# Optimization experiments

Measured on AMD Instinct MI355X. Metric: run time of the kernel, lower is better.

## Reference

```python
import jax, jax.numpy as jnp
import numpy as np

B, NQ, NKV = 4, 1024, 2048
Q_DIM = K_DIM = V_DIM = 1024
HEADS, DIM_HEAD = 16, 64
INNER = HEADS * DIM_HEAD


def setup_inputs() -> dict:
    key = jax.random.key(0)
    ks = jax.random.split(key, 10)
    return {
        "x": jax.random.normal(ks[0], (B, NQ, Q_DIM), dtype=jnp.float32),
        "key_t": jax.random.normal(ks[1], (B, NKV, K_DIM), dtype=jnp.float32),
        "value": jax.random.normal(ks[2], (B, NKV, V_DIM), dtype=jnp.float32),
        "mask": jax.random.randint(ks[3], (B, NQ, NKV), 0, 2) == 1,
        "Wq": jax.random.normal(ks[4], (Q_DIM, INNER), dtype=jnp.float32) * (Q_DIM ** -0.5),
        "Wk": jax.random.normal(ks[5], (K_DIM, INNER), dtype=jnp.float32) * (K_DIM ** -0.5),
        "Wv": jax.random.normal(ks[6], (V_DIM, INNER), dtype=jnp.float32) * (V_DIM ** -0.5),
        "Wo": jax.random.normal(ks[7], (INNER, Q_DIM), dtype=jnp.float32) * (INNER ** -0.5),
        "gamma": jnp.ones((Q_DIM,), dtype=jnp.float32),
        "beta": jnp.zeros((Q_DIM,), dtype=jnp.float32),
    }


def reference(x, key_t, value, mask, Wq, Wk, Wv, Wo, gamma, beta):
    # LayerNorm over last dim
    mu = jnp.mean(x, axis=-1, keepdims=True)
    var = jnp.var(x, axis=-1, keepdims=True)
    xn = (x - mu) * jax.lax.rsqrt(var + 1e-5) * gamma + beta

    h, d = HEADS, DIM_HEAD
    # b n (h d) -> b h n d
    q = (xn @ Wq).reshape(B, NQ, h, d).transpose(0, 2, 1, 3)
    k = (key_t @ Wk).reshape(B, NKV, h, d).transpose(0, 2, 1, 3)
    v = (value @ Wv).reshape(B, NKV, h, d).transpose(0, 2, 1, 3)

    scale = d ** -0.5
    dots = jnp.einsum("bhnd,bhmd->bhnm", q, k) * scale  # [b,h,nq,nkv]
    min_neg = -jnp.finfo(dots.dtype).max
    dots = jnp.where(mask[:, None, :, :], min_neg, dots)
    attn = jax.nn.softmax(dots, axis=-1)
    out = jnp.einsum("bhnm,bhmd->bhnd", attn, v)
    out = out.transpose(0, 2, 1, 3).reshape(B, NQ, INNER)  # b h n d -> b n (h d)
    return out @ Wo
```

## Files before the change

kernel.cpp:

```cpp
#include <hip/hip_runtime.h>

typedef unsigned short u16;
typedef unsigned int u32;
typedef unsigned char u8;

typedef __attribute__((ext_vector_type(8))) short bf16x8;
typedef __attribute__((ext_vector_type(4))) short bf16x4;
typedef __attribute__((ext_vector_type(4))) float f32x4;

__device__ __forceinline__ float bf2f(u16 u) {
    union { u32 i; float f; } v; v.i = ((u32)u) << 16; return v.f;
}
__device__ __forceinline__ u16 f2bf(float f) {
    union { float f; u32 i; } v; v.f = f;
    u32 r = v.i + 0x7fffu + ((v.i >> 16) & 1u);
    return (u16)(r >> 16);
}
__device__ __forceinline__ u32 pkbf(float a, float b) {
    return (u32)f2bf(a) | ((u32)f2bf(b) << 16);
}
__device__ __forceinline__ float fexp2(float x) { return __builtin_amdgcn_exp2f(x); }

__device__ __forceinline__ void async16(u16* lds, const u16* g) {
    __builtin_amdgcn_global_load_lds(
        (const __attribute__((address_space(1))) void*)g,
        (__attribute__((address_space(3))) void*)lds, 16, 0, 0);
}

__global__ __launch_bounds__(256) void detect_dtype(const u32* __restrict__ x,
                                                    int* __restrict__ flag) {
    int tid = threadIdx.x;
    int hits = 0;
    for (int i = 0; i < 4; ++i) {
        u32 w = x[tid * 4 + i];
        u32 e = (w >> 7) & 0xFFu;
        hits += (e >= 110u && e <= 131u) ? 1 : 0;
    }
    for (int off = 1; off < 64; off <<= 1) hits += __shfl_xor(hits, off, 64);
    __shared__ int red[4];
    int wave = tid >> 6, lane = tid & 63;
    if (lane == 0) red[wave] = hits;
    __syncthreads();
    if (tid == 0) flag[0] = (red[0] + red[1] + red[2] + red[3] > 512) ? 1 : 0;
}

__global__ __launch_bounds__(256) void conv_bf16_2(const void* __restrict__ src0,
                                                   const void* __restrict__ src1,
                                                   u16* __restrict__ dst0,
                                                   u16* __restrict__ dst1,
                                                   const int* __restrict__ flagp,
                                                   int half_blocks) {
    int flag = *flagp;
    const void* src = (blockIdx.x < (u32)half_blocks) ? src0 : src1;
    u16* dst = (blockIdx.x < (u32)half_blocks) ? dst0 : dst1;
    int blk = (blockIdx.x < (u32)half_blocks) ? blockIdx.x : (blockIdx.x - half_blocks);
    size_t i = (size_t)blk * 256 + threadIdx.x;
    if (flag) {
        ((uint4*)dst)[i] = ((const uint4*)src)[i];
    } else {
        const float4* s = (const float4*)src + i * 2;
        float4 f0 = s[0], f1 = s[1];
        u16 t[8];
        t[0] = f2bf(f0.x); t[1] = f2bf(f0.y); t[2] = f2bf(f0.z); t[3] = f2bf(f0.w);
        t[4] = f2bf(f1.x); t[5] = f2bf(f1.y); t[6] = f2bf(f1.z); t[7] = f2bf(f1.w);
        ((uint4*)dst)[i] = *(const uint4*)t;
    }
}

__global__ __launch_bounds__(256) void mask_pack(const int* __restrict__ m,
                                                 u8* __restrict__ o) {
    size_t i = (size_t)blockIdx.x * 256 + threadIdx.x;
    const int4* mp = (const int4*)m + i * 4;
    uint4 out;
    u32* op = (u32*)&out;
    for (int j = 0; j < 4; ++j) {
        int4 a = mp[j];
        op[j] = (a.x == 0 ? 0xFFu : 0u) | (a.y == 0 ? 0xFF00u : 0u) |
                (a.z == 0 ? 0xFF0000u : 0u) | (a.w == 0 ? 0xFF000000u : 0u);
    }
    ((uint4*)o)[i] = out;
}

__global__ __launch_bounds__(256) void ln_kernel(const void* __restrict__ x_,
                                                 const void* __restrict__ g_,
                                                 const void* __restrict__ b_,
                                                 u16* __restrict__ out,
                                                 const int* __restrict__ flagp) {
    int flag = *flagp;
    int row = blockIdx.x;
    int tid = threadIdx.x;
    float v[4];
    if (flag) {
        const u16* xr = (const u16*)x_ + (size_t)row * 1024;
        uint2 d = *(const uint2*)&xr[tid * 4];
        v[0] = bf2f((u16)(d.x & 0xffff));
        v[1] = bf2f((u16)(d.x >> 16));
        v[2] = bf2f((u16)(d.y & 0xffff));
        v[3] = bf2f((u16)(d.y >> 16));
    } else {
        const float* xr = (const float*)x_ + (size_t)row * 1024;
        float4 d = *(const float4*)&xr[tid * 4];
        v[0] = d.x; v[1] = d.y; v[2] = d.z; v[3] = d.w;
    }
    float s  = v[0] + v[1] + v[2] + v[3];
    float ss = v[0]*v[0] + v[1]*v[1] + v[2]*v[2] + v[3]*v[3];
    for (int off = 1; off < 64; off <<= 1) {
        s  += __shfl_xor(s,  off, 64);
        ss += __shfl_xor(ss, off, 64);
    }
    __shared__ float red[8];
    int wave = tid >> 6, lane = tid & 63;
    if (lane == 0) { red[wave] = s; red[4 + wave] = ss; }
    __syncthreads();
    s  = red[0] + red[1] + red[2] + red[3];
    ss = red[4] + red[5] + red[6] + red[7];
    float mu   = s * (1.0f / 1024.0f);
    float var  = ss * (1.0f / 1024.0f) - mu * mu;
    float rstd = rsqrtf(var + 1e-5f);
    u16 r01[4];
    for (int j = 0; j < 4; ++j) {
        float g, bb;
        if (flag) { g = bf2f(((const u16*)g_)[tid * 4 + j]); bb = bf2f(((const u16*)b_)[tid * 4 + j]); }
        else      { g = ((const float*)g_)[tid * 4 + j];     bb = ((const float*)b_)[tid * 4 + j]; }
        r01[j] = f2bf((v[j] - mu) * rstd * g + bb);
    }
    uint2 o;
    o.x = (u32)r01[0] | ((u32)r01[1] << 16);
    o.y = (u32)r01[2] | ((u32)r01[3] << 16);
    *(uint2*)&out[(size_t)row * 1024 + tid * 4] = o;
}

__global__ __launch_bounds__(256) void transpose64x4(const void* __restrict__ s0,
                                                     const void* __restrict__ s1,
                                                     const void* __restrict__ s2,
                                                     const void* __restrict__ s3,
                                                     u16* __restrict__ d0,
                                                     u16* __restrict__ d1,
                                                     u16* __restrict__ d2,
                                                     u16* __restrict__ d3,
                                                     int rows, int cols,
                                                     const int* __restrict__ flagp) {
    __shared__ u16 t[64][65];
    int flag = *flagp;
    const void* src_ = (blockIdx.z == 0) ? s0 : (blockIdx.z == 1) ? s1 :
                       (blockIdx.z == 2) ? s2 : s3;
    u16* dst = (blockIdx.z == 0) ? d0 : (blockIdx.z == 1) ? d1 :
               (blockIdx.z == 2) ? d2 : d3;
    int bx = blockIdx.x * 64;
    int by = blockIdx.y * 64;
    int tid = threadIdx.x;
    for (int i = 0; i < 16; ++i) {
        int r = i * 4 + (tid >> 6);
        int c = tid & 63;
        size_t idx = (size_t)(by + r) * cols + bx + c;
        t[r][c] = flag ? ((const u16*)src_)[idx] : f2bf(((const float*)src_)[idx]);
    }
    __syncthreads();
    for (int i = 0; i < 16; ++i) {
        int r = i * 4 + (tid >> 6);
        int c = tid & 63;
        dst[(size_t)(bx + r) * rows + by + c] = t[c][r];
    }
}

__global__ __launch_bounds__(256, 2) void gemm128(const u16* __restrict__ A,
                                                  const u16* __restrict__ Bt,
                                                  void* __restrict__ C_,
                                                  int M, int N, int K,
                                                  const int* __restrict__ flagp,
                                                  int c_flagged, float cscale,
                                                  int vt_mode, int mdiv) {
    __shared__ u16 As[128 * 64];
    __shared__ u16 Bs[128 * 64];
    int flag = *flagp;
    bool c_bf16 = c_flagged ? (flag != 0) : true;

    int id  = blockIdx.x;
    int j   = id >> 3;
    int gy  = (id & 7) + 8 * (j % mdiv);
    int bnt = j / mdiv;

    int tid  = threadIdx.x;
    int wave = tid >> 6, lane = tid & 63;
    int quad = lane >> 4, l16 = lane & 15;
    size_t bm = (size_t)gy * 128;
    size_t bn = (size_t)bnt * 128;
    int wm = (wave >> 1) * 64, wn = (wave & 1) * 64;

    int lr  = lane >> 3;
    int csw = (lane & 7) ^ lr;
    const u16* Ag = A  + (bm + wave * 32 + lr) * (size_t)K + csw * 8;
    const u16* Bg = Bt + (bn + wave * 32 + lr) * (size_t)K + csw * 8;
    u16* Al = &As[(wave * 32) * 64];
    u16* Bl = &Bs[(wave * 32) * 64];

    f32x4 acc[4][4];
#pragma unroll
    for (int i = 0; i < 4; ++i)
#pragma unroll
        for (int jj = 0; jj < 4; ++jj)
            acc[i][jj] = (f32x4){0.f, 0.f, 0.f, 0.f};

    int rsw = l16 & 7;

    for (int k0 = 0; k0 < K; k0 += 64) {
        __syncthreads();
#pragma unroll
        for (int i = 0; i < 4; ++i) {
            async16(Al + i * 8 * 64, Ag + (size_t)i * 8 * K + k0);
            async16(Bl + i * 8 * 64, Bg + (size_t)i * 8 * K + k0);
        }
        __syncthreads();

#pragma unroll
        for (int ks = 0; ks < 2; ++ks) {
            int chunk = ((ks << 2) | quad) ^ rsw;
            bf16x8 af[4], bfr[4];
#pragma unroll
            for (int mi = 0; mi < 4; ++mi)
                af[mi]  = *(const bf16x8*)&As[(wm + mi * 16 + l16) * 64 + chunk * 8];
#pragma unroll
            for (int ni = 0; ni < 4; ++ni)
                bfr[ni] = *(const bf16x8*)&Bs[(wn + ni * 16 + l16) * 64 + chunk * 8];
#pragma unroll
            for (int mi = 0; mi < 4; ++mi)
#pragma unroll
                for (int ni = 0; ni < 4; ++ni)
                    acc[mi][ni] = __builtin_amdgcn_mfma_f32_16x16x32_bf16(
                        af[mi], bfr[ni], acc[mi][ni], 0, 0, 0);
        }
    }

    if (vt_mode) {
        u16* C = (u16*)C_;
#pragma unroll
        for (int mi = 0; mi < 4; ++mi)
#pragma unroll
            for (int ni = 0; ni < 4; ++ni) {
                size_t m = bm + wm + mi * 16 + quad * 4;
                size_t n = bn + wn + ni * 16 + l16;
                size_t bb = m >> 11, kv = m & 2047;
                size_t hh = n >> 6,  d  = n & 63;
                u16 t4[4];
#pragma unroll
                for (int r = 0; r < 4; ++r) t4[r] = f2bf(acc[mi][ni][r]);
                *(uint2*)&C[((bb * 16 + hh) * 64 + d) * 2048 + kv] = *(const uint2*)t4;
            }
    } else {
#pragma unroll
        for (int mi = 0; mi < 4; ++mi)
#pragma unroll
            for (int ni = 0; ni < 4; ++ni)
#pragma unroll
                for (int r = 0; r < 4; ++r) {
                    size_t row = bm + wm + mi * 16 + quad * 4 + r;
                    size_t col = bn + wn + ni * 16 + l16;
                    float val = acc[mi][ni][r] * cscale;
                    if (c_bf16) ((u16*)C_)[row * N + col]   = f2bf(val);
                    else        ((float*)C_)[row * N + col] = val;
                }
    }
}

__global__ __launch_bounds__(256) void attn_kernel(const u16* __restrict__ qg,
                                                   const u16* __restrict__ kg,
                                                   const u16* __restrict__ vtg,
                                                   const u8* __restrict__ masku,
                                                   u16* __restrict__ og) {
    __shared__ u16 Ks[64 * 64];
    __shared__ u16 Vst[64 * 64];

    const int NQc = 1024, NKVc = 2048, HD = 1024;
    int id = blockIdx.x;
    int j  = id >> 3;
    int qt = j >> 3;
    int g  = (id & 7) + ((j & 7) << 3);
    int h  = g & 15;
    int b  = g >> 4;

    int tid  = threadIdx.x;
    int wave = tid >> 6, lane = tid & 63;
    int quad = lane >> 4, l16 = lane & 15;
    int q0 = qt * 64;

    const u16* qrow = qg + ((size_t)b * NQc + q0 + wave * 16 + l16) * HD + h * 64;
    bf16x8 aq0 = *(const bf16x8*)&qrow[quad * 8];
    bf16x8 aq1 = *(const bf16x8*)&qrow[32 + quad * 8];

    int lr  = lane >> 3;
    int csw = (lane & 7) ^ lr;
    const u16* kbase = kg  + ((size_t)b * NKVc + wave * 8 + lr) * HD + h * 64 + csw * 8;
    const u16* vbase = vtg + (((size_t)b * 16 + h) * 64 + wave * 8 + lr) * (size_t)NKVc + csw * 8;
    u16* kl = Ks  + (wave * 8) * 64;
    u16* vl = Vst + (wave * 8) * 64;

    f32x4 O[4], lacc;
#pragma unroll
    for (int dt = 0; dt < 4; ++dt) O[dt] = (f32x4){0.f, 0.f, 0.f, 0.f};
    lacc = (f32x4){0.f, 0.f, 0.f, 0.f};

    bf16x4 ones4;
#pragma unroll
    for (int jj = 0; jj < 4; ++jj) ones4[jj] = (short)0x3F80;

    const u8* mrow = masku + ((size_t)b * NQc + q0 + wave * 16 + l16) * (size_t)NKVc;

    int l7 = l16 & 7;

    for (int kv0 = 0; kv0 < NKVc; kv0 += 64) {
        __syncthreads();
#pragma unroll
        for (int i = 0; i < 2; ++i) {
            async16(kl + i * 32 * 64, kbase + ((size_t)kv0 + i * 32) * HD);
            async16(vl + i * 32 * 64, vbase + (size_t)(i * 32) * NKVc + kv0);
        }
        __syncthreads();

        bf16x4 pfr[4];
#pragma unroll
        for (int nt = 0; nt < 4; ++nt) {
            const u16* krow = Ks + (nt * 16 + l16) * 64;
            bf16x8 bk0 = *(const bf16x8*)&krow[(quad ^ l7) * 8];
            bf16x8 bk1 = *(const bf16x8*)&krow[((4 + quad) ^ l7) * 8];
            f32x4 st = (f32x4){0.f, 0.f, 0.f, 0.f};
            st = __builtin_amdgcn_mfma_f32_16x16x32_bf16(bk0, aq0, st, 0, 0, 0);
            st = __builtin_amdgcn_mfma_f32_16x16x32_bf16(bk1, aq1, st, 0, 0, 0);

            u32 mword = *(const u32*)&mrow[kv0 + nt * 16 + quad * 4];
            u32 p01 = pkbf(fexp2(st[0]), fexp2(st[1])) &
                      __builtin_amdgcn_perm(0u, mword, 0x01010000u);
            u32 p23 = pkbf(fexp2(st[2]), fexp2(st[3])) &
                      __builtin_amdgcn_perm(0u, mword, 0x03030202u);
            uint2 pu; pu.x = p01; pu.y = p23;
            pfr[nt] = *(const bf16x4*)&pu;

            lacc = __builtin_amdgcn_mfma_f32_16x16x16bf16_1k(ones4, pfr[nt], lacc, 0, 0, 0);
        }

#pragma unroll
        for (int dt = 0; dt < 4; ++dt) {
            const u16* vrow = Vst + (dt * 16 + l16) * 64;
#pragma unroll
            for (int kvs = 0; kvs < 4; ++kvs) {
                int gran = ((kvs << 1) | (quad >> 1)) ^ l7;
                bf16x4 av = *(const bf16x4*)&vrow[gran * 8 + (quad & 1) * 4];
                O[dt] = __builtin_amdgcn_mfma_f32_16x16x16bf16_1k(av, pfr[kvs], O[dt], 0, 0, 0);
            }
        }
    }

    float inv = 1.0f / lacc[0];
    u16* orow = og + ((size_t)b * NQc + q0 + wave * 16 + l16) * HD + h * 64;
#pragma unroll
    for (int dt = 0; dt < 4; ++dt) {
        u16 t4[4];
#pragma unroll
        for (int r = 0; r < 4; ++r) t4[r] = f2bf(O[dt][r] * inv);
        *(uint2*)&orow[dt * 16 + quad * 4] = *(const uint2*)t4;
    }
}

extern "C" void kernel_launch(void* const* d_in, const int* in_sizes, int n_in,
                              void* d_out, int out_size, void* d_ws, size_t ws_size,
                              hipStream_t stream) {
    const void* x     = d_in[0];
    const void* key   = d_in[1];
    const void* value = d_in[2];
    const int*  mask  = (const int*)d_in[3];
    const void* Wq    = d_in[4];
    const void* Wk    = d_in[5];
    const void* Wv    = d_in[6];
    const void* Wo    = d_in[7];
    const void* gamma = d_in[8];
    const void* beta  = d_in[9];

    char* ws = (char*)d_ws;
    int* flag = (int*)(ws);
    u16* xn  = (u16*)(ws + ( 1ull << 20));
    u8*  mu8 = (u8*) (ws + ( 1ull << 20));
    u16* q   = (u16*)(ws + ( 9ull << 20));
    u16* kb  = (u16*)(ws + ( 9ull << 20));
    u16* ao  = (u16*)(ws + (17ull << 20));
    u16* k   = (u16*)(ws + (25ull << 20));
    u16* vb  = (u16*)(ws + (25ull << 20));
    u16* vT  = (u16*)(ws + (41ull << 20));
    u16* Wqt = (u16*)(ws + (57ull << 20));
    u16* Wkt = (u16*)(ws + (59ull << 20));
    u16* Wvt = (u16*)(ws + (61ull << 20));
    u16* Wot = (u16*)(ws + (63ull << 20));

    const float QSCALE = 0.125f * 1.44269504f;

    detect_dtype<<<1, 256, 0, stream>>>((const u32*)x, flag);

    ln_kernel<<<4096, 256, 0, stream>>>(x, gamma, beta, xn, flag);

    dim3 tg4(16, 16, 4);
    transpose64x4<<<tg4, 256, 0, stream>>>(Wq, Wk, Wv, Wo, Wqt, Wkt, Wvt, Wot,
                                           1024, 1024, flag);

    conv_bf16_2<<<8192, 256, 0, stream>>>(key, value, kb, vb, flag, 4096);

    gemm128<<<512, 256, 0, stream>>>(vb, Wvt, vT, 8192, 1024, 1024, flag, 0, 1.0f, 1, 8);
    gemm128<<<512, 256, 0, stream>>>(kb, Wkt, k,  8192, 1024, 1024, flag, 0, 1.0f, 0, 8);
    gemm128<<<256, 256, 0, stream>>>(xn, Wqt, q,  4096, 1024, 1024, flag, 0, QSCALE, 0, 4);

    mask_pack<<<2048, 256, 0, stream>>>(mask, mu8);

    attn_kernel<<<1024, 256, 0, stream>>>(q, k, vT, mu8, ao);

    gemm128<<<256, 256, 0, stream>>>(ao, Wot, d_out, 4096, 1024, 1024, flag, 1, 1.0f, 0, 4);
}
```

Before: 361.3 us.

## Split attention KV range across two blocks and bit-pack the mask

```diff
diff --git a/kernel.cpp b/kernel.cpp
--- a/kernel.cpp
+++ b/kernel.cpp
@@ -3,6 +3,7 @@
 typedef unsigned short u16;
 typedef unsigned int u32;
 typedef unsigned char u8;
+typedef unsigned long long u64;
 
 typedef __attribute__((ext_vector_type(8))) short bf16x8;
 typedef __attribute__((ext_vector_type(4))) short bf16x4;
@@ -67,18 +68,21 @@
     }
 }
 
-__global__ __launch_bounds__(256) void mask_pack(const int* __restrict__ m,
-                                                 u8* __restrict__ o) {
-    size_t i = (size_t)blockIdx.x * 256 + threadIdx.x;
-    const int4* mp = (const int4*)m + i * 4;
-    uint4 out;
-    u32* op = (u32*)&out;
-    for (int j = 0; j < 4; ++j) {
-        int4 a = mp[j];
-        op[j] = (a.x == 0 ? 0xFFu : 0u) | (a.y == 0 ? 0xFF00u : 0u) |
-                (a.z == 0 ? 0xFF0000u : 0u) | (a.w == 0 ? 0xFF000000u : 0u);
-    }
-    ((uint4*)o)[i] = out;
+__global__ __launch_bounds__(256) void mask_bits(const int* __restrict__ m,
+                                                 u64* __restrict__ o) {
+    int wid  = (blockIdx.x * 256 + threadIdx.x) >> 6;
+    int lane = threadIdx.x & 63;
+    size_t base = (size_t)wid * 2048;
+    for (int it = 0; it < 8; ++it) {
+        u64 b0 = __ballot(m[base + it * 256 +   0 + lane] == 0);
+        u64 b1 = __ballot(m[base + it * 256 +  64 + lane] == 0);
+        u64 b2 = __ballot(m[base + it * 256 + 128 + lane] == 0);
+        u64 b3 = __ballot(m[base + it * 256 + 192 + lane] == 0);
+        if (lane == 0) {
+            size_t idx = (base + it * 256) >> 6;
+            o[idx + 0] = b0; o[idx + 1] = b1; o[idx + 2] = b2; o[idx + 3] = b3;
+        }
+    }
 }
 
 __global__ __launch_bounds__(256) void ln_kernel(const void* __restrict__ x_,
@@ -265,15 +269,23 @@
 __global__ __launch_bounds__(256) void attn_kernel(const u16* __restrict__ qg,
                                                    const u16* __restrict__ kg,
                                                    const u16* __restrict__ vtg,
-                                                   const u8* __restrict__ masku,
-                                                   u16* __restrict__ og) {
+                                                   const u32* __restrict__ mbits,
+                                                   float* __restrict__ o0,
+                                                   float* __restrict__ o1b0,
+                                                   float* __restrict__ o1b1,
+                                                   float* __restrict__ o1b2,
+                                                   float* __restrict__ o1b3,
+                                                   float* __restrict__ lacc0,
+                                                   float* __restrict__ lacc1) {
     __shared__ u16 Ks[64 * 64];
     __shared__ u16 Vst[64 * 64];
 
     const int NQc = 1024, NKVc = 2048, HD = 1024;
     int id = blockIdx.x;
     int j  = id >> 3;
-    int qt = j >> 3;
+    int qt2 = j >> 3;
+    int half = qt2 >> 4;
+    int qt = qt2 & 15;
     int g  = (id & 7) + ((j & 7) << 3);
     int h  = g & 15;
     int b  = g >> 4;
@@ -303,11 +315,12 @@
 #pragma unroll
     for (int jj = 0; jj < 4; ++jj) ones4[jj] = (short)0x3F80;
 
-    const u8* mrow = masku + ((size_t)b * NQc + q0 + wave * 16 + l16) * (size_t)NKVc;
+    const u32* mrowb = mbits + ((size_t)b * NQc + q0 + wave * 16 + l16) * 64;
 
     int l7 = l16 & 7;
-
-    for (int kv0 = 0; kv0 < NKVc; kv0 += 64) {
+    int kvbeg = half << 10;
+
+    for (int kv0 = kvbeg; kv0 < kvbeg + 1024; kv0 += 64) {
         __syncthreads();
 #pragma unroll
         for (int i = 0; i < 2; ++i) {
@@ -315,6 +328,8 @@
             async16(vl + i * 32 * 64, vbase + (size_t)(i * 32) * NKVc + kv0);
         }
         __syncthreads();
+
+        uint2 bw = *(const uint2*)&mrowb[kv0 >> 5];
 
         bf16x4 pfr[4];
 #pragma unroll
@@ -326,11 +341,12 @@
             st = __builtin_amdgcn_mfma_f32_16x16x32_bf16(bk0, aq0, st, 0, 0, 0);
             st = __builtin_amdgcn_mfma_f32_16x16x32_bf16(bk1, aq1, st, 0, 0, 0);
 
-            u32 mword = *(const u32*)&mrow[kv0 + nt * 16 + quad * 4];
-            u32 p01 = pkbf(fexp2(st[0]), fexp2(st[1])) &
-                      __builtin_amdgcn_perm(0u, mword, 0x01010000u);
-            u32 p23 = pkbf(fexp2(st[2]), fexp2(st[3])) &
-                      __builtin_amdgcn_perm(0u, mword, 0x03030202u);
+            u32 w  = (nt < 2) ? bw.x : bw.y;
+            u32 m4 = (w >> (((nt & 1) << 4) + (quad << 2))) & 0xFu;
+            u32 m01 = ((m4 & 1u) ? 0xFFFFu : 0u) | ((m4 & 2u) ? 0xFFFF0000u : 0u);
+            u32 m23 = ((m4 & 4u) ? 0xFFFFu : 0u) | ((m4 & 8u) ? 0xFFFF0000u : 0u);
+            u32 p01 = pkbf(fexp2(st[0]), fexp2(st[1])) & m01;
+            u32 p23 = pkbf(fexp2(st[2]), fexp2(st[3])) & m23;
             uint2 pu; pu.x = p01; pu.y = p23;
             pfr[nt] = *(const bf16x4*)&pu;
 
@@ -349,15 +365,40 @@
         }
     }
 
-    float inv = 1.0f / lacc[0];
-    u16* orow = og + ((size_t)b * NQc + q0 + wave * 16 + l16) * HD + h * 64;
-#pragma unroll
-    for (int dt = 0; dt < 4; ++dt) {
-        u16 t4[4];
-#pragma unroll
-        for (int r = 0; r < 4; ++r) t4[r] = f2bf(O[dt][r] * inv);
-        *(uint2*)&orow[dt * 16 + quad * 4] = *(const uint2*)t4;
-    }
+    int qi = q0 + wave * 16 + l16;
+    float* opart = half ? (b == 0 ? o1b0 : b == 1 ? o1b1 : b == 2 ? o1b2 : o1b3) : o0;
+    size_t rbase = half ? (size_t)qi : ((size_t)b * NQc + qi);
+    float* orow = opart + rbase * 1024 + h * 64;
+#pragma unroll
+    for (int dt = 0; dt < 4; ++dt)
+        *(float4*)&orow[dt * 16 + quad * 4] = (float4){O[dt][0], O[dt][1], O[dt][2], O[dt][3]};
+
+    float* lp = half ? lacc1 : lacc0;
+    if (quad == 0) lp[((size_t)b * 16 + h) * 1024 + qi] = lacc[0];
+}
+
+__global__ __launch_bounds__(256) void combine_halves(const float* __restrict__ p0,
+                                                      const float* __restrict__ p1b0,
+                                                      const float* __restrict__ p1b1,
+                                                      const float* __restrict__ p1b2,
+                                                      const float* __restrict__ p1b3,
+                                                      const float* __restrict__ l0,
+                                                      const float* __restrict__ l1,
+                                                      u16* __restrict__ ao) {
+    int row = blockIdx.x;
+    int b = row >> 10, qq = row & 1023;
+    const float* p1 = (b == 0) ? p1b0 : (b == 1) ? p1b1 : (b == 2) ? p1b2 : p1b3;
+    int tid = threadIdx.x;
+    int hd = tid * 4;
+    int h  = hd >> 6;
+    float4 a = *(const float4*)&p0[(size_t)row * 1024 + hd];
+    float4 c = *(const float4*)&p1[(size_t)qq  * 1024 + hd];
+    size_t li = ((size_t)b * 16 + h) * 1024 + qq;
+    float inv = 1.0f / (l0[li] + l1[li]);
+    uint2 o;
+    o.x = (u32)f2bf((a.x + c.x) * inv) | ((u32)f2bf((a.y + c.y) * inv) << 16);
+    o.y = (u32)f2bf((a.z + c.z) * inv) | ((u32)f2bf((a.w + c.w) * inv) << 16);
+    *(uint2*)&ao[(size_t)row * 1024 + hd] = o;
 }
 
 extern "C" void kernel_launch(void* const* d_in, const int* in_sizes, int n_in,
@@ -376,18 +417,25 @@
 
     char* ws = (char*)d_ws;
     int* flag = (int*)(ws);
-    u16* xn  = (u16*)(ws + ( 1ull << 20));
-    u8*  mu8 = (u8*) (ws + ( 1ull << 20));
-    u16* q   = (u16*)(ws + ( 9ull << 20));
-    u16* kb  = (u16*)(ws + ( 9ull << 20));
-    u16* ao  = (u16*)(ws + (17ull << 20));
-    u16* k   = (u16*)(ws + (25ull << 20));
-    u16* vb  = (u16*)(ws + (25ull << 20));
-    u16* vT  = (u16*)(ws + (41ull << 20));
-    u16* Wqt = (u16*)(ws + (57ull << 20));
-    u16* Wkt = (u16*)(ws + (59ull << 20));
-    u16* Wvt = (u16*)(ws + (61ull << 20));
-    u16* Wot = (u16*)(ws + (63ull << 20));
+    u16* xn   = (u16*)(ws + ( 1ull << 20));
+    u32* mbits= (u32*)(ws + ( 1ull << 20));
+    float* o1b0 = (float*)(ws + ( 2ull << 20));
+    float* la0  = (float*)(ws + ( 6ull << 20));
+    float* la1  = (float*)(ws + ( 6ull << 20) + (256ull << 10));
+    u16* q    = (u16*)(ws + ( 9ull << 20));
+    u16* kb   = (u16*)(ws + ( 9ull << 20));
+    u16* ao   = (u16*)(ws + ( 9ull << 20));
+    float* o1b1 = (float*)(ws + (17ull << 20));
+    float* o1b2 = (float*)(ws + (21ull << 20));
+    u16* k    = (u16*)(ws + (25ull << 20));
+    u16* vb   = (u16*)(ws + (25ull << 20));
+    u16* vT   = (u16*)(ws + (41ull << 20));
+    u16* Wqt  = (u16*)(ws + (57ull << 20));
+    float* o1b3 = (float*)(ws + (57ull << 20));
+    u16* Wkt  = (u16*)(ws + (59ull << 20));
+    u16* Wvt  = (u16*)(ws + (61ull << 20));
+    u16* Wot  = (u16*)(ws + (63ull << 20));
+    float* o0 = (float*)d_out;
 
     const float QSCALE = 0.125f * 1.44269504f;
 
@@ -405,9 +453,13 @@
     gemm128<<<512, 256, 0, stream>>>(kb, Wkt, k,  8192, 1024, 1024, flag, 0, 1.0f, 0, 8);
     gemm128<<<256, 256, 0, stream>>>(xn, Wqt, q,  4096, 1024, 1024, flag, 0, QSCALE, 0, 4);
 
-    mask_pack<<<2048, 256, 0, stream>>>(mask, mu8);
-
-    attn_kernel<<<1024, 256, 0, stream>>>(q, k, vT, mu8, ao);
+    mask_bits<<<1024, 256, 0, stream>>>(mask, (u64*)mbits);
+
+    attn_kernel<<<2048, 256, 0, stream>>>(q, k, vT, mbits,
+                                          o0, o1b0, o1b1, o1b2, o1b3, la0, la1);
+
+    combine_halves<<<4096, 256, 0, stream>>>(o0, o1b0, o1b1, o1b2, o1b3,
+                                             la0, la1, ao);
 
     gemm128<<<256, 256, 0, stream>>>(ao, Wot, d_out, 4096, 1024, 1024, flag, 1, 1.0f, 0, 4);
 }
```

Result: faster. 352.5 us (-2.4%).
